# Optimization experiments

Measured on AMD Instinct MI355X. Metric: run time of the kernel, lower is better.

## Reference

```python
import jax, jax.numpy as jnp
import numpy as np

# E2M1 (FP4) representable magnitudes and rounding midpoints
LEVELS = jnp.array([0.0, 0.5, 1.0, 1.5, 2.0, 3.0, 4.0, 6.0], dtype=jnp.float32)
BOUNDS = jnp.array([0.25, 0.75, 1.25, 1.75, 2.5, 3.5, 5.0], dtype=jnp.float32)
E2M1_MAX = 6.0
EPS = 1e-12


def e2m1_block_quant_dequant(x, block_size):
    """Block-wise E2M1 fake-quantization along the last dim.

    Per block of `block_size` elements: scale = absmax / 6.0, then
    round-to-nearest onto the E2M1 grid {0,.5,1,1.5,2,3,4,6} (signed)
    and dequantize. Returns (dequantized x, per-block scales).
    """
    shape = x.shape
    nb = shape[-1] // block_size
    xb = x.reshape(*shape[:-1], nb, block_size)
    amax = jnp.max(jnp.abs(xb), axis=-1, keepdims=True)          # [..., nb, 1]
    scale = jnp.maximum(amax / E2M1_MAX, EPS)
    v = xb / scale
    mag = jnp.abs(v)
    # nearest E2M1 level: count how many rounding boundaries |v| exceeds
    idx = jnp.sum((mag[..., None] > BOUNDS).astype(jnp.int32), axis=-1)
    q = jnp.sign(v) * LEVELS[idx] * scale                        # dequantized
    return q.reshape(shape), scale[..., 0]


def setup_inputs() -> dict:
    key = jax.random.key(0)
    k1, k2, k3 = jax.random.split(key, 3)
    x = jax.random.normal(k1, (8, 1500, 1280), dtype=jnp.float32)
    weight = jax.random.normal(k2, (5120, 1280), dtype=jnp.float32) * 0.02
    bias = jax.random.normal(k3, (5120,), dtype=jnp.float32) * 0.01
    return {"x": x, "weight": weight, "bias": bias}


def reference(x, weight, bias):
    # activation quant (block_size_act = 32, along feature dim)
    x_q, _ = e2m1_block_quant_dequant(x, 32)
    # weight quant (block_size_w = 32, along in_features dim)
    w_q, scale_w = e2m1_block_quant_dequant(weight, 32)
    # F.linear: x @ W^T + b
    out = jnp.einsum('bsi,oi->bso', x_q, w_q) + bias
    return (out, scale_w)
```

## Files before the change

kernel.cpp:

```cpp
#include <hip/hip_runtime.h>
#include <hip/hip_fp16.h>


typedef _Float16 f16;
typedef _Float16 f16x8 __attribute__((ext_vector_type(8)));
typedef float f32x4 __attribute__((ext_vector_type(4)));

#define M_ROWS 12000
#define M_PAD  12032
#define N_COLS 5120
#define K_DIM  1280
#define KB     40
#define NTN    20

#define BAR()   asm volatile("s_barrier" ::: "memory")
#define LGKM(N) asm volatile("s_waitcnt lgkmcnt(%0)" :: "i"(N) : "memory")
#define VMCNT(N) asm volatile("s_waitcnt vmcnt(%0)" :: "i"(N) : "memory")
#define SB0()   __builtin_amdgcn_sched_barrier(0)
#define GLDS(gp, lp) __builtin_amdgcn_global_load_lds( \
    (const __attribute__((address_space(1))) unsigned*)(gp), \
    (__attribute__((address_space(3))) unsigned*)(lp), 16, 0, 0)

__device__ __forceinline__ float e2m1_level(float a) {
    float lv;
    if (a > 2.5f)       lv = (a > 3.5f) ? ((a > 5.0f) ? 6.0f : 4.0f) : 3.0f;
    else if (a > 1.25f) lv = (a > 1.75f) ? 2.0f : 1.5f;
    else                lv = (a > 0.75f) ? 1.0f : ((a > 0.25f) ? 0.5f : 0.0f);
    return lv;
}

__global__ __launch_bounds__(256) void quant_x_kernel(const float* __restrict__ x,
                                                      f16* __restrict__ xq) {
    int t = blockIdx.x * blockDim.x + threadIdx.x;
    int row = t / 160;
    int c8  = t % 160;
    f16x8 o;
    if (row < M_ROWS) {
        const float* p = x + (size_t)row * K_DIM + c8 * 8;
        float v[8];
        *(float4*)&v[0] = *(const float4*)p;
        *(float4*)&v[4] = *(const float4*)(p + 4);
        float am = 0.0f;
        #pragma unroll
        for (int i = 0; i < 8; ++i) am = fmaxf(am, fabsf(v[i]));
        am = fmaxf(am, __shfl_xor(am, 1));
        am = fmaxf(am, __shfl_xor(am, 2));
        float scale = fmaxf(am / 6.0f, 1e-12f);
        #pragma unroll
        for (int i = 0; i < 8; ++i) {
            float tq = v[i] / scale;
            float q  = copysignf(e2m1_level(fabsf(tq)), tq) * scale;
            o[i] = (f16)q;
        }
    } else {
        #pragma unroll
        for (int i = 0; i < 8; ++i) o[i] = (f16)0.0f;
    }
    *(f16x8*)(xq + (size_t)row * K_DIM + c8 * 8) = o;
}

__global__ __launch_bounds__(256) void quant_w_kernel(const float* __restrict__ w,
                                                      f16* __restrict__ wq,
                                                      float* __restrict__ scale_out) {
    int t = blockIdx.x * blockDim.x + threadIdx.x;
    int row = t / 160;
    int c8  = t % 160;
    const float* p = w + (size_t)row * K_DIM + c8 * 8;
    float v[8];
    *(float4*)&v[0] = *(const float4*)p;
    *(float4*)&v[4] = *(const float4*)(p + 4);
    float am = 0.0f;
    #pragma unroll
    for (int i = 0; i < 8; ++i) am = fmaxf(am, fabsf(v[i]));
    am = fmaxf(am, __shfl_xor(am, 1));
    am = fmaxf(am, __shfl_xor(am, 2));
    float scale = fmaxf(am / 6.0f, 1e-12f);
    if ((t & 3) == 0) scale_out[row * KB + (c8 >> 2)] = scale;
    f16x8 o;
    #pragma unroll
    for (int i = 0; i < 8; ++i) {
        float tq = v[i] / scale;
        float q  = copysignf(e2m1_level(fabsf(tq)), tq) * scale;
        o[i] = (f16)q;
    }
    *(f16x8*)(wq + (size_t)row * K_DIM + c8 * 8) = o;
}


__device__ __forceinline__ void stage_half(const f16* __restrict__ g, f16* l, int tid) {
    #pragma unroll
    for (int s = 0; s < 2; ++s) {
        int j = s * 512 + tid;
        int r = j >> 3;
        int c = (j & 7) ^ (r & 7);
        GLDS(g + (size_t)r * K_DIM + c * 8, l + (size_t)j * 8);
    }
}

#define READ_A(dst, buf, rbase)                                                \
    _Pragma("unroll")                                                          \
    for (int fm = 0; fm < 4; ++fm) {                                           \
        dst[fm][0] = *(const f16x8*)&(buf)[((rbase) + fm * 16) * 64 + swz[0]]; \
        dst[fm][1] = *(const f16x8*)&(buf)[((rbase) + fm * 16) * 64 + swz[1]]; \
    }
#define READ_B(dst, buf, rbase)                                                \
    _Pragma("unroll")                                                          \
    for (int fn = 0; fn < 2; ++fn) {                                           \
        dst[fn][0] = *(const f16x8*)&(buf)[((rbase) + fn * 16) * 64 + swz[0]]; \
        dst[fn][1] = *(const f16x8*)&(buf)[((rbase) + fn * 16) * 64 + swz[1]]; \
    }
#define MFMA_Q(ma, mb, mo, no)                                                 \
    __builtin_amdgcn_s_setprio(1);                                             \
    _Pragma("unroll")                                                          \
    for (int fm = 0; fm < 4; ++fm)                                             \
        _Pragma("unroll")                                                      \
        for (int fn = 0; fn < 2; ++fn) {                                       \
            acc[fm + mo][fn + no] = __builtin_amdgcn_mfma_f32_16x16x32_f16(    \
                ma[fm][0], mb[fn][0], acc[fm + mo][fn + no], 0, 0, 0);         \
            acc[fm + mo][fn + no] = __builtin_amdgcn_mfma_f32_16x16x32_f16(    \
                ma[fm][1], mb[fn][1], acc[fm + mo][fn + no], 0, 0, 0);         \
        }                                                                      \
    __builtin_amdgcn_s_setprio(0);

template<bool SREST, int V4>
__device__ __forceinline__ void iter8(f16* A0, f16* B0, f16* A1, f16* B1,
                                      const f16* gA1, const f16* gA2,
                                      const f16* gB2, const f16* gB3,
                                      f32x4 (&acc)[8][4],
                                      int tid, int arow0, int brow0, const int (&swz)[2]) {
    f16x8 aLO[4][2], aHI[4][2], bLO[2][2], bHI[2][2];

    READ_A(aLO, A0, arow0);
    READ_B(bLO, B0, brow0);
    stage_half(gA1, A1, tid);
    LGKM(8);
    BAR();
    LGKM(0); SB0();
    MFMA_Q(aLO, bLO, 0, 0);
    BAR();
    READ_B(bHI, B0, brow0 + 32);
    stage_half(gA1 + 128 * K_DIM, A1 + 8192, tid);
    BAR();
    LGKM(0); SB0();
    MFMA_Q(aLO, bHI, 0, 2);
    BAR();
    READ_A(aHI, A0, arow0 + 64);
    if (SREST) stage_half(gB2, B0, tid);
    BAR();
    LGKM(0); SB0();
    MFMA_Q(aHI, bHI, 4, 2);
    BAR();
    if (SREST) stage_half(gA2, A0, tid);
    BAR();
    MFMA_Q(aHI, bLO, 4, 0);
    VMCNT(V4);
    BAR();
    READ_A(aLO, A1, arow0);
    READ_B(bLO, B1, brow0);
    if (SREST) stage_half(gA2 + 128 * K_DIM, A0 + 8192, tid);
    LGKM(8);
    BAR();
    LGKM(0); SB0();
    MFMA_Q(aLO, bLO, 0, 0);
    BAR();
    READ_B(bHI, B1, brow0 + 32);
    if (SREST) stage_half(gB2 + 128 * K_DIM, B0 + 8192, tid);
    BAR();
    LGKM(0); SB0();
    MFMA_Q(aLO, bHI, 0, 2);
    BAR();
    READ_A(aHI, A1, arow0 + 64);
    if (SREST) stage_half(gB3, B1, tid);
    BAR();
    LGKM(0); SB0();
    MFMA_Q(aHI, bHI, 4, 2);
    BAR();
    if (SREST) stage_half(gB3 + 128 * K_DIM, B1 + 8192, tid);
    BAR();
    MFMA_Q(aHI, bLO, 4, 0);
    if (SREST) VMCNT(4);
    BAR();
}

__global__ __launch_bounds__(512, 2) void gemm_kernel(const f16* __restrict__ A,
                                                      const f16* __restrict__ B,
                                                      const float* __restrict__ bias,
                                                      float* __restrict__ C) {
    extern __shared__ f16 sm[];
    int mt = blockIdx.x / NTN;
    int nt = blockIdx.x % NTN;

    int tid  = threadIdx.x;
    int lane = tid & 63;
    int wid  = tid >> 6;
    int wr   = wid >> 2;
    int wc   = wid & 3;
    int l15  = lane & 15;

    int swz[2] = { (((lane >> 4)    ) ^ (lane & 7)) * 8,
                   (((lane >> 4) + 4) ^ (lane & 7)) * 8 };
    int arow0 = wr * 128 + l15;
    int brow0 = wc * 64 + l15;

    const f16* gAb = A + (size_t)(mt * 256) * K_DIM;
    const f16* gBb = B + (size_t)(nt * 256) * K_DIM;

    f16* A0 = sm;
    f16* B0 = sm + 16384;
    f16* A1 = sm + 32768;
    f16* B1 = sm + 49152;

    f32x4 acc[8][4] = {};

    stage_half(gBb,               B0,        tid);
    stage_half(gAb,               A0,        tid);
    stage_half(gAb + 128 * K_DIM, A0 + 8192, tid);
    stage_half(gBb + 128 * K_DIM, B0 + 8192, tid);
    stage_half(gBb + 64,               B1,        tid);
    stage_half(gBb + 64 + 128 * K_DIM, B1 + 8192, tid);
    VMCNT(4);
    BAR();

    for (int i = 0; i < 9; ++i) {
        const f16* gA1 = gAb + (2 * i + 1) * 64;
        const f16* gA2 = gAb + (2 * i + 2) * 64;
        const f16* gB2 = gBb + (2 * i + 2) * 64;
        const f16* gB3 = gBb + (2 * i + 3) * 64;
        iter8<true, 4>(A0, B0, A1, B1, gA1, gA2, gB2, gB3,
                       acc, tid, arow0, brow0, swz);
    }
    iter8<false, 0>(A0, B0, A1, B1, gAb + 19 * 64, gAb, gBb, gBb,
                    acc, tid, arow0, brow0, swz);

    int crow0 = mt * 256 + wr * 128;
    int ccol  = nt * 256 + wc * 64 + l15;
    float bz[4];
    #pragma unroll
    for (int fn = 0; fn < 4; ++fn) bz[fn] = bias[ccol + fn * 16];

    #pragma unroll
    for (int fm = 0; fm < 8; ++fm) {
        #pragma unroll
        for (int j = 0; j < 4; ++j) {
            int row = crow0 + fm * 16 + (lane >> 4) * 4 + j;
            if (row < M_ROWS) {
                float* cp = C + (size_t)row * N_COLS + ccol;
                #pragma unroll
                for (int fn = 0; fn < 4; ++fn)
                    cp[fn * 16] = acc[fm][fn][j] + bz[fn];
            }
        }
    }
}

extern "C" void kernel_launch(void* const* d_in, const int* in_sizes, int n_in,
                              void* d_out, int out_size, void* d_ws, size_t ws_size,
                              hipStream_t stream) {
    const float* x      = (const float*)d_in[0];
    const float* weight = (const float*)d_in[1];
    const float* bias   = (const float*)d_in[2];
    float* out     = (float*)d_out;
    float* scale_w = (float*)d_out + (size_t)M_ROWS * N_COLS;

    f16* xq = (f16*)d_ws;
    f16* wq = (f16*)((char*)d_ws + (size_t)M_PAD * K_DIM * sizeof(f16));

    (void)hipFuncSetAttribute((const void*)gemm_kernel,
                              hipFuncAttributeMaxDynamicSharedMemorySize, 131072);

    {
        int threads = M_PAD * (K_DIM / 8);
        quant_x_kernel<<<threads / 256, 256, 0, stream>>>(x, xq);
    }
    {
        int threads = N_COLS * (K_DIM / 8);
        quant_w_kernel<<<threads / 256, 256, 0, stream>>>(weight, wq, scale_w);
    }
    {
        int grid = (M_PAD / 256) * (N_COLS / 256);
        gemm_kernel<<<grid, 512, 131072, stream>>>(xq, wq, bias, out);
    }
}
```

Measured before the change: 198.0 us.

## Fuse quant kernels, remap GEMM tiles per XCD, drop explicit LDS waits

Merges the activation and weight quantization into one launch using a block-index split, removing one kernel launch. Remaps GEMM workgroup ids so that each XCD processes a contiguous range of tiles, aiming to improve L2 reuse of A/B tiles. Removes the explicit lgkmcnt waits, sched barriers and several s_barriers in the main loop, and issues global-to-LDS staging before the LDS reads. The compiler then inserts its own waits, which risks losing the hand-tuned overlap and creates a possible LDS hazard if the removed barriers were guarding buffer reuse.

```diff
diff --git a/kernel.cpp b/kernel.cpp
--- a/kernel.cpp
+++ b/kernel.cpp
@@ -12,11 +12,10 @@
 #define K_DIM  1280
 #define KB     40
 #define NTN    20
+#define XBLK   7520
 
 #define BAR()   asm volatile("s_barrier" ::: "memory")
-#define LGKM(N) asm volatile("s_waitcnt lgkmcnt(%0)" :: "i"(N) : "memory")
 #define VMCNT(N) asm volatile("s_waitcnt vmcnt(%0)" :: "i"(N) : "memory")
-#define SB0()   __builtin_amdgcn_sched_barrier(0)
 #define GLDS(gp, lp) __builtin_amdgcn_global_load_lds( \
     (const __attribute__((address_space(1))) unsigned*)(gp), \
     (__attribute__((address_space(3))) unsigned*)(lp), 16, 0, 0)
@@ -29,14 +28,44 @@
     return lv;
 }
 
-__global__ __launch_bounds__(256) void quant_x_kernel(const float* __restrict__ x,
-                                                      f16* __restrict__ xq) {
-    int t = blockIdx.x * blockDim.x + threadIdx.x;
-    int row = t / 160;
-    int c8  = t % 160;
-    f16x8 o;
-    if (row < M_ROWS) {
-        const float* p = x + (size_t)row * K_DIM + c8 * 8;
+__global__ __launch_bounds__(256) void quant_fused(const float* __restrict__ x,
+                                                   f16* __restrict__ xq,
+                                                   const float* __restrict__ w,
+                                                   f16* __restrict__ wq,
+                                                   float* __restrict__ scale_out) {
+    int b = blockIdx.x;
+    if (b < XBLK) {
+        int t = b * 256 + threadIdx.x;
+        int row = t / 160;
+        int c8  = t % 160;
+        f16x8 o;
+        if (row < M_ROWS) {
+            const float* p = x + (size_t)row * K_DIM + c8 * 8;
+            float v[8];
+            *(float4*)&v[0] = *(const float4*)p;
+            *(float4*)&v[4] = *(const float4*)(p + 4);
+            float am = 0.0f;
+            #pragma unroll
+            for (int i = 0; i < 8; ++i) am = fmaxf(am, fabsf(v[i]));
+            am = fmaxf(am, __shfl_xor(am, 1));
+            am = fmaxf(am, __shfl_xor(am, 2));
+            float scale = fmaxf(am / 6.0f, 1e-12f);
+            #pragma unroll
+            for (int i = 0; i < 8; ++i) {
+                float tq = v[i] / scale;
+                float q  = copysignf(e2m1_level(fabsf(tq)), tq) * scale;
+                o[i] = (f16)q;
+            }
+        } else {
+            #pragma unroll
+            for (int i = 0; i < 8; ++i) o[i] = (f16)0.0f;
+        }
+        *(f16x8*)(xq + (size_t)row * K_DIM + c8 * 8) = o;
+    } else {
+        int t = (b - XBLK) * 256 + threadIdx.x;
+        int row = t / 160;
+        int c8  = t % 160;
+        const float* p = w + (size_t)row * K_DIM + c8 * 8;
         float v[8];
         *(float4*)&v[0] = *(const float4*)p;
         *(float4*)&v[4] = *(const float4*)(p + 4);
@@ -46,44 +75,16 @@
         am = fmaxf(am, __shfl_xor(am, 1));
         am = fmaxf(am, __shfl_xor(am, 2));
         float scale = fmaxf(am / 6.0f, 1e-12f);
+        if ((t & 3) == 0) scale_out[row * KB + (c8 >> 2)] = scale;
+        f16x8 o;
         #pragma unroll
         for (int i = 0; i < 8; ++i) {
             float tq = v[i] / scale;
             float q  = copysignf(e2m1_level(fabsf(tq)), tq) * scale;
             o[i] = (f16)q;
         }
-    } else {
-        #pragma unroll
-        for (int i = 0; i < 8; ++i) o[i] = (f16)0.0f;
-    }
-    *(f16x8*)(xq + (size_t)row * K_DIM + c8 * 8) = o;
-}
-
-__global__ __launch_bounds__(256) void quant_w_kernel(const float* __restrict__ w,
-                                                      f16* __restrict__ wq,
-                                                      float* __restrict__ scale_out) {
-    int t = blockIdx.x * blockDim.x + threadIdx.x;
-    int row = t / 160;
-    int c8  = t % 160;
-    const float* p = w + (size_t)row * K_DIM + c8 * 8;
-    float v[8];
-    *(float4*)&v[0] = *(const float4*)p;
-    *(float4*)&v[4] = *(const float4*)(p + 4);
-    float am = 0.0f;
-    #pragma unroll
-    for (int i = 0; i < 8; ++i) am = fmaxf(am, fabsf(v[i]));
-    am = fmaxf(am, __shfl_xor(am, 1));
-    am = fmaxf(am, __shfl_xor(am, 2));
-    float scale = fmaxf(am / 6.0f, 1e-12f);
-    if ((t & 3) == 0) scale_out[row * KB + (c8 >> 2)] = scale;
-    f16x8 o;
-    #pragma unroll
-    for (int i = 0; i < 8; ++i) {
-        float tq = v[i] / scale;
-        float q  = copysignf(e2m1_level(fabsf(tq)), tq) * scale;
-        o[i] = (f16)q;
-    }
-    *(f16x8*)(wq + (size_t)row * K_DIM + c8 * 8) = o;
+        *(f16x8*)(wq + (size_t)row * K_DIM + c8 * 8) = o;
+    }
 }
 
 
@@ -130,53 +131,37 @@
                                       int tid, int arow0, int brow0, const int (&swz)[2]) {
     f16x8 aLO[4][2], aHI[4][2], bLO[2][2], bHI[2][2];
 
+    stage_half(gA1, A1, tid);
     READ_A(aLO, A0, arow0);
     READ_B(bLO, B0, brow0);
-    stage_half(gA1, A1, tid);
-    LGKM(8);
-    BAR();
-    LGKM(0); SB0();
     MFMA_Q(aLO, bLO, 0, 0);
     BAR();
+    stage_half(gA1 + 128 * K_DIM, A1 + 8192, tid);
     READ_B(bHI, B0, brow0 + 32);
-    stage_half(gA1 + 128 * K_DIM, A1 + 8192, tid);
-    BAR();
-    LGKM(0); SB0();
     MFMA_Q(aLO, bHI, 0, 2);
     BAR();
+    if (SREST) stage_half(gB2, B0, tid);
     READ_A(aHI, A0, arow0 + 64);
-    if (SREST) stage_half(gB2, B0, tid);
-    BAR();
-    LGKM(0); SB0();
     MFMA_Q(aHI, bHI, 4, 2);
     BAR();
     if (SREST) stage_half(gA2, A0, tid);
-    BAR();
     MFMA_Q(aHI, bLO, 4, 0);
     VMCNT(V4);
     BAR();
+    if (SREST) stage_half(gA2 + 128 * K_DIM, A0 + 8192, tid);
     READ_A(aLO, A1, arow0);
     READ_B(bLO, B1, brow0);
-    if (SREST) stage_half(gA2 + 128 * K_DIM, A0 + 8192, tid);
-    LGKM(8);
-    BAR();
-    LGKM(0); SB0();
     MFMA_Q(aLO, bLO, 0, 0);
     BAR();
+    if (SREST) stage_half(gB2 + 128 * K_DIM, B0 + 8192, tid);
     READ_B(bHI, B1, brow0 + 32);
-    if (SREST) stage_half(gB2 + 128 * K_DIM, B0 + 8192, tid);
-    BAR();
-    LGKM(0); SB0();
     MFMA_Q(aLO, bHI, 0, 2);
     BAR();
+    if (SREST) stage_half(gB3, B1, tid);
     READ_A(aHI, A1, arow0 + 64);
-    if (SREST) stage_half(gB3, B1, tid);
-    BAR();
-    LGKM(0); SB0();
     MFMA_Q(aHI, bHI, 4, 2);
     BAR();
     if (SREST) stage_half(gB3 + 128 * K_DIM, B1 + 8192, tid);
-    BAR();
     MFMA_Q(aHI, bLO, 4, 0);
     if (SREST) VMCNT(4);
     BAR();
@@ -187,8 +172,13 @@
                                                       const float* __restrict__ bias,
                                                       float* __restrict__ C) {
     extern __shared__ f16 sm[];
-    int mt = blockIdx.x / NTN;
-    int nt = blockIdx.x % NTN;
+
+    int orig = blockIdx.x;
+    int xcd  = orig & 7;
+    int loc  = orig >> 3;
+    int wgid = (xcd < 4 ? xcd * 118 : 472 + (xcd - 4) * 117) + loc;
+    int mt = wgid / NTN;
+    int nt = wgid % NTN;
 
     int tid  = threadIdx.x;
     int lane = tid & 63;
@@ -269,12 +259,8 @@
                               hipFuncAttributeMaxDynamicSharedMemorySize, 131072);
 
     {
-        int threads = M_PAD * (K_DIM / 8);
-        quant_x_kernel<<<threads / 256, 256, 0, stream>>>(x, xq);
-    }
-    {
-        int threads = N_COLS * (K_DIM / 8);
-        quant_w_kernel<<<threads / 256, 256, 0, stream>>>(weight, wq, scale_w);
+        int wblocks = N_COLS * (K_DIM / 8) / 256;
+        quant_fused<<<XBLK + wblocks, 256, 0, stream>>>(x, xq, weight, wq, scale_w);
     }
     {
         int grid = (M_PAD / 256) * (N_COLS / 256);
```

Measured after the change: 193.9 us. 2.1% less time.
